# Optimization experiments

Hardware: AMD Instinct MI355X
Metric: run time of the kernel (lower is better)

The kernel has to match this reference:

```python
import jax, jax.numpy as jnp
import numpy as np

NUM_HEADS = 8
SR = 8
EPS = 1e-5


def _ln(x, g, b):
    m = jnp.mean(x, axis=-1, keepdims=True)
    v = jnp.mean((x - m) ** 2, axis=-1, keepdims=True)
    return (x - m) * jax.lax.rsqrt(v + EPS) * g + b


def _conv(x, w, b, stride, pad, groups=1):
    y = jax.lax.conv_general_dilated(
        x, w, (stride, stride), ((pad, pad), (pad, pad)),
        feature_group_count=groups,
        dimension_numbers=('NCHW', 'OIHW', 'NCHW'))
    return y + b[None, :, None, None]


def setup_inputs() -> dict:
    key = jax.random.key(0)
    ks = jax.random.split(key, 12)
    B, H, W, C = 2, 128, 128, 128
    N = H * W
    Ch = C // 2

    def nrm(k, shape, std=0.02):
        return jax.random.normal(k, shape, jnp.float32) * std

    return dict(
        x=jax.random.normal(ks[0], (B, N, C), jnp.float32),
        q_w=nrm(ks[1], (C, C)),
        sr1_w=nrm(ks[2], (C, C, 8, 8), float(np.sqrt(2.0 / (8 * 8 * C)))),
        sr1_b=jnp.zeros((C,), jnp.float32),
        norm1_g=jnp.ones((C,), jnp.float32),
        norm1_b=jnp.zeros((C,), jnp.float32),
        sr2_w=nrm(ks[3], (C, C, 4, 4), float(np.sqrt(2.0 / (4 * 4 * C)))),
        sr2_b=jnp.zeros((C,), jnp.float32),
        norm2_g=jnp.ones((C,), jnp.float32),
        norm2_b=jnp.zeros((C,), jnp.float32),
        kv1_w=nrm(ks[4], (C, C)),
        kv2_w=nrm(ks[5], (C, C)),
        lc1_w=nrm(ks[6], (Ch, 1, 3, 3), float(np.sqrt(2.0 / 9))),
        lc1_b=jnp.zeros((Ch,), jnp.float32),
        lc2_w=nrm(ks[7], (Ch, 1, 3, 3), float(np.sqrt(2.0 / 9))),
        lc2_b=jnp.zeros((Ch,), jnp.float32),
        proj_w=nrm(ks[8], (C, C)),
        proj_b=jnp.zeros((C,), jnp.float32),
        H=H, W=W,
    )


def reference(x, q_w, sr1_w, sr1_b, norm1_g, norm1_b, sr2_w, sr2_b, norm2_g,
              norm2_b, kv1_w, kv2_w, lc1_w, lc1_b, lc2_w, lc2_b, proj_w,
              proj_b, H, W):
    B, N, C = x.shape
    h = NUM_HEADS
    hd = C // h
    hh = h // 2
    Ch = C // 2
    scale = hd ** (-0.5)

    # q: (B, h, N, hd)
    q = (x @ q_w.T).reshape(B, N, h, hd).transpose(0, 2, 1, 3)
    x_img = x.transpose(0, 2, 1).reshape(B, C, H, W)

    def branch(q_half, sr_w, sr_b, ng, nb, kv_w, lc_w, lc_b, k_sr, hk, wk):
        # spatial reduction conv (kernel == stride == k_sr)
        xr = _conv(x_img, sr_w, sr_b, k_sr, 0)            # (B, C, hk, wk)
        Nk = hk * wk
        xr = xr.reshape(B, C, Nk).transpose(0, 2, 1)       # (B, Nk, C)
        xr = jax.nn.gelu(_ln(xr, ng, nb), approximate=False)
        kv = (xr @ kv_w.T).reshape(B, Nk, 2, hh, hd).transpose(2, 0, 3, 1, 4)
        k_, v_ = kv[0], kv[1]                              # (B, hh, Nk, hd)
        attn = jax.nn.softmax(
            jnp.einsum('bhqd,bhkd->bhqk', q_half, k_) * scale, axis=-1)
        # depthwise local conv fused into V
        v_img = v_.transpose(0, 2, 1, 3).reshape(B, Nk, Ch)
        v_img = v_img.transpose(0, 2, 1).reshape(B, Ch, hk, wk)
        loc = _conv(v_img, lc_w, lc_b, 1, 1, groups=Ch)
        loc = loc.reshape(B, Ch, Nk).reshape(B, hh, hd, Nk).transpose(0, 1, 3, 2)
        v_ = v_ + loc
        out = jnp.einsum('bhqk,bhkd->bhqd', attn, v_)      # (B, hh, N, hd)
        return out.transpose(0, 2, 1, 3).reshape(B, N, Ch)

    x1 = branch(q[:, :hh], sr1_w, sr1_b, norm1_g, norm1_b, kv1_w, lc1_w,
                lc1_b, SR, H // SR, W // SR)
    x2 = branch(q[:, hh:], sr2_w, sr2_b, norm2_g, norm2_b, kv2_w, lc2_w,
                lc2_b, SR // 2, H * 2 // SR, W * 2 // SR)
    out = jnp.concatenate([x1, x2], axis=-1) @ proj_w.T + proj_b
    return out
```

## Files before the change

kernel.cpp:

```cpp
#include <hip/hip_runtime.h>
#include <math.h>


typedef __attribute__((ext_vector_type(8))) short bf16x8;
typedef __attribute__((ext_vector_type(4))) float f32x4;

__device__ inline unsigned short f2bf(float f) {
  unsigned int u = __builtin_bit_cast(unsigned int, f);
  u = (u + 0x7FFFu + ((u >> 16) & 1u)) >> 16;
  return (unsigned short)u;
}

__global__ void k_cvt(const float* __restrict__ in, unsigned short* __restrict__ o, int n8) {
  int t = blockIdx.x * 256 + threadIdx.x;
  if (t >= n8) return;
  const float4 a = ((const float4*)in)[t * 2];
  const float4 b = ((const float4*)in)[t * 2 + 1];
  ((ushort4*)o)[t * 2]     = make_ushort4(f2bf(a.x), f2bf(a.y), f2bf(a.z), f2bf(a.w));
  ((ushort4*)o)[t * 2 + 1] = make_ushort4(f2bf(b.x), f2bf(b.y), f2bf(b.z), f2bf(b.w));
}

__global__ void k_cvtw4(const float* w0, const float* w1, const float* w2, const float* w3,
                        unsigned short* o0, unsigned short* o1, unsigned short* o2, unsigned short* o3) {
  const float* s; unsigned short* d;
  switch (blockIdx.y) {
    case 0: s = w0; d = o0; break;
    case 1: s = w1; d = o1; break;
    case 2: s = w2; d = o2; break;
    default: s = w3; d = o3; break;
  }
  int t = blockIdx.x * 256 + threadIdx.x;
  const float4 a = ((const float4*)s)[t * 2];
  const float4 b = ((const float4*)s)[t * 2 + 1];
  ((ushort4*)d)[t * 2]     = make_ushort4(f2bf(a.x), f2bf(a.y), f2bf(a.z), f2bf(a.w));
  ((ushort4*)d)[t * 2 + 1] = make_ushort4(f2bf(b.x), f2bf(b.y), f2bf(b.z), f2bf(b.w));
}

template <int KLOG, int SSLOG>
__global__ void k_convw(const float* __restrict__ w, unsigned short* __restrict__ o) {
  int idx = blockIdx.x * 256 + threadIdx.x;
  int k = idx & ((1 << KLOG) - 1), n = idx >> KLOG;
  int c_in = k & 127, kpos = k >> 7;
  o[idx] = f2bf(w[(n << KLOG) + (c_in << SSLOG) + kpos]);
}

template <int S, bool SPLITK, bool OUTBF, bool BIAS>
__global__ void __launch_bounds__(256)
k_mgemm(const void* __restrict__ Ap, const unsigned short* __restrict__ Bw,
        const float* __restrict__ bias, void* __restrict__ outp,
        int M, int K, int Kc) {
  constexpr int WK = (S == 8) ? 16 : 32;
  constexpr int WLOG = (S == 8) ? 4 : 5;
  constexpr int PSH = (S == 8) ? 8 : 10;
  constexpr int SLOG = (S == 8) ? 3 : 2;

  __shared__ unsigned short As[128][72];
  __shared__ unsigned short Bs[128][72];

  const int tid = threadIdx.x;
  const int lane = tid & 63, wv = tid >> 6;
  const int lq = lane & 15, g = lane >> 4;
  const int wr = wv >> 1, wc = wv & 1;
  const int m0 = blockIdx.x * 128;
  int k_begin = 0, k_end = K;
  if (SPLITK) { k_begin = blockIdx.y * Kc; k_end = k_begin + Kc; }

  const f32x4 zf = {0.f, 0.f, 0.f, 0.f};
  f32x4 acc[4][4];
#pragma unroll
  for (int i = 0; i < 4; ++i)
#pragma unroll
    for (int j = 0; j < 4; ++j) acc[i][j] = zf;

  for (int k0 = k_begin; k0 < k_end; k0 += 64) {
    __syncthreads();
    if constexpr (S == 0) {
      const unsigned short* Ab = (const unsigned short*)Ap;
      int mrow = tid >> 3, kk = (tid & 7) * 8;
#pragma unroll
      for (int p = 0; p < 4; ++p) {
        int m = p * 32 + mrow;
        *(bf16x8*)&As[m][kk] = *(const bf16x8*)(Ab + (size_t)(m0 + m) * K + k0 + kk);
      }
    } else {
      const float* xg = (const float*)Ap;
      int mrow = tid >> 4, kk = (tid & 15) * 4;
      int kgl = k0 + kk;
      int c_in = kgl & 127, kpos = kgl >> 7;
      int ky = kpos >> SLOG, kx = kpos & (S - 1);
#pragma unroll
      for (int p = 0; p < 8; ++p) {
        int m = p * 16 + mrow;
        int r = m0 + m;
        int pix = r & ((1 << PSH) - 1), bb = r >> PSH;
        int oy = pix >> WLOG, ox = pix & (WK - 1);
        int y = oy * S + ky, xx = ox * S + kx;
        const float4 v = *(const float4*)(xg + ((size_t)((bb << 14) + (y << 7) + xx) << 7) + c_in);
        *(ushort4*)&As[m][kk] = make_ushort4(f2bf(v.x), f2bf(v.y), f2bf(v.z), f2bf(v.w));
      }
    }
    {
      int nrow = tid >> 3, kk = (tid & 7) * 8;
#pragma unroll
      for (int p = 0; p < 4; ++p) {
        int n = p * 32 + nrow;
        *(bf16x8*)&Bs[n][kk] = *(const bf16x8*)(Bw + (size_t)n * K + k0 + kk);
      }
    }
    __syncthreads();
#pragma unroll
    for (int kk = 0; kk < 64; kk += 32) {
      bf16x8 af[4], bfr[4];
#pragma unroll
      for (int i = 0; i < 4; ++i) {
        af[i]  = *(const bf16x8*)&As[wr * 64 + i * 16 + lq][kk + g * 8];
        bfr[i] = *(const bf16x8*)&Bs[wc * 64 + i * 16 + lq][kk + g * 8];
      }
#pragma unroll
      for (int i = 0; i < 4; ++i)
#pragma unroll
        for (int j = 0; j < 4; ++j)
          acc[i][j] = __builtin_amdgcn_mfma_f32_16x16x32_bf16(af[i], bfr[j], acc[i][j], 0, 0, 0);
    }
  }

  size_t obase = 0;
  if (SPLITK) obase = (size_t)blockIdx.y * M * 128;
#pragma unroll
  for (int i = 0; i < 4; ++i) {
#pragma unroll
    for (int j = 0; j < 4; ++j) {
      int col = wc * 64 + j * 16 + lq;
      float bv = BIAS ? bias[col] : 0.f;
#pragma unroll
      for (int r = 0; r < 4; ++r) {
        int row = m0 + wr * 64 + i * 16 + g * 4 + r;
        float v = acc[i][j][r] + bv;
        if (OUTBF) ((unsigned short*)outp)[obase + (size_t)row * 128 + col] = f2bf(v);
        else       ((float*)outp)[obase + (size_t)row * 128 + col] = v;
      }
    }
  }
}

__global__ void __launch_bounds__(128)
k_ln_gelu(const float* __restrict__ part, int SK, int Mstride,
          const float* __restrict__ cb, const float* __restrict__ g,
          const float* __restrict__ b, unsigned short* __restrict__ out) {
  __shared__ float red[2];
  __shared__ float red2[2];
  int row = blockIdx.x;
  int t = threadIdx.x;
  const float* p = part + (size_t)row * 128 + t;
  float v = 0.f;
  for (int sk = 0; sk < SK; ++sk) v += p[(size_t)sk * Mstride];
  v += cb[t];

  float s = v;
#pragma unroll
  for (int o = 32; o > 0; o >>= 1) s += __shfl_down(s, o);
  if ((t & 63) == 0) red[t >> 6] = s;
  __syncthreads();
  float mean = (red[0] + red[1]) * (1.f / 128.f);

  float d = v - mean;
  float s2 = d * d;
#pragma unroll
  for (int o = 32; o > 0; o >>= 1) s2 += __shfl_down(s2, o);
  if ((t & 63) == 0) red2[t >> 6] = s2;
  __syncthreads();
  float var = (red2[0] + red2[1]) * (1.f / 128.f);

  float y = d * rsqrtf(var + 1e-5f) * g[t] + b[t];
  out[(size_t)row * 128 + t] = f2bf(y * 0.5f * (1.f + erff(y * 0.70710678118654752f)));
}

template <int WK>
__global__ void __launch_bounds__(256)
k_locconv(const float* __restrict__ kvb, const float* __restrict__ lw,
          const float* __restrict__ lb, float* __restrict__ vf) {
  constexpr int LOG = (WK == 16) ? 4 : 5;
  int idx = blockIdx.x * 256 + threadIdx.x;
  int c = idx & 63;
  int r = idx >> 6;
  int x = r & (WK - 1);
  int t2 = r >> LOG;
  int y = t2 & (WK - 1);
  int b = t2 >> LOG;
  const float* base = kvb + ((size_t)b * WK * WK) * 128 + 64 + c;
  float a = lb[c];
#pragma unroll
  for (int dy = -1; dy <= 1; ++dy) {
    int yy = y + dy;
    if (yy < 0 || yy >= WK) continue;
#pragma unroll
    for (int dx = -1; dx <= 1; ++dx) {
      int xx = x + dx;
      if (xx < 0 || xx >= WK) continue;
      a += base[(yy * WK + xx) * 128] * lw[c * 9 + (dy + 1) * 3 + (dx + 1)];
    }
  }
  vf[(size_t)r * 64 + c] = base[(y * WK + x) * 128] + a;
}

__global__ void __launch_bounds__(256)
k_mattn(const unsigned short* __restrict__ qb, const float* __restrict__ kvb,
        const float* __restrict__ vfb, unsigned short* __restrict__ concat,
        int NK, int h0) {
  __shared__ unsigned short Ks[64][24];
  __shared__ unsigned short Vt[16][72];
  __shared__ unsigned short Pl[4][16][40];

  const int tid = threadIdx.x;
  const int lane = tid & 63, wv = tid >> 6;
  const int lq = lane & 15, g = lane >> 4;
  const int lh = blockIdx.y, b = blockIdx.z;
  const int qbase = blockIdx.x * 64 + wv * 16;
  const int kcol = lh * 16;
  const int ocol = (h0 + lh) * 16;
  const size_t bNK = (size_t)b * NK;

  const bf16x8 kz = {0, 0, 0, 0, 0, 0, 0, 0};
  const f32x4 zf = {0.f, 0.f, 0.f, 0.f};

  bf16x8 qf = kz;
  if (g < 2)
    qf = *(const bf16x8*)(qb + ((size_t)b * 16384 + qbase + lq) * 128 + ocol + g * 8);

  f32x4 acc = zf;
  float m = -1e30f, l = 0.f;

  for (int key0 = 0; key0 < NK; key0 += 64) {
    __syncthreads();
    {
      int key = tid >> 2, hdc = (tid & 3) * 4;
      const float4 kf = *(const float4*)(kvb + (bNK + key0 + key) * 128 + kcol + hdc);
      *(ushort4*)&Ks[key][hdc] = make_ushort4(f2bf(kf.x * 0.25f), f2bf(kf.y * 0.25f),
                                              f2bf(kf.z * 0.25f), f2bf(kf.w * 0.25f));
    }
    {
      int d = tid & 15, kc = (tid >> 4) * 4;
      const float* vp = vfb + (bNK + key0 + kc) * 64 + kcol + d;
      *(ushort4*)&Vt[d][kc] = make_ushort4(f2bf(vp[0]), f2bf(vp[64]),
                                           f2bf(vp[128]), f2bf(vp[192]));
    }
    __syncthreads();

#pragma unroll
    for (int half = 0; half < 2; ++half) {
      bf16x8 k0f = kz, k1f = kz;
      if (g < 2) {
        k0f = *(const bf16x8*)&Ks[half * 32 + lq][g * 8];
        k1f = *(const bf16x8*)&Ks[half * 32 + 16 + lq][g * 8];
      }
      f32x4 c0 = __builtin_amdgcn_mfma_f32_16x16x32_bf16(k0f, qf, zf, 0, 0, 0);
      f32x4 c1 = __builtin_amdgcn_mfma_f32_16x16x32_bf16(k1f, qf, zf, 0, 0, 0);

      float tmax = fmaxf(fmaxf(fmaxf(c0[0], c0[1]), fmaxf(c0[2], c0[3])),
                         fmaxf(fmaxf(c1[0], c1[1]), fmaxf(c1[2], c1[3])));
      tmax = fmaxf(tmax, __shfl_xor(tmax, 16));
      tmax = fmaxf(tmax, __shfl_xor(tmax, 32));
      float mnew = fmaxf(m, tmax);
      float corr = __expf(m - mnew);
      float p0[4], p1[4], ls = 0.f;
#pragma unroll
      for (int r = 0; r < 4; ++r) {
        p0[r] = __expf(c0[r] - mnew);
        p1[r] = __expf(c1[r] - mnew);
        ls += p0[r] + p1[r];
      }
      ls += __shfl_xor(ls, 16);
      ls += __shfl_xor(ls, 32);
      l = l * corr + ls;
      m = mnew;
      acc = acc * corr;

      *(ushort2*)&Pl[wv][lq][g * 4]          = make_ushort2(f2bf(p0[0]), f2bf(p0[1]));
      *(ushort2*)&Pl[wv][lq][g * 4 + 2]      = make_ushort2(f2bf(p0[2]), f2bf(p0[3]));
      *(ushort2*)&Pl[wv][lq][16 + g * 4]     = make_ushort2(f2bf(p1[0]), f2bf(p1[1]));
      *(ushort2*)&Pl[wv][lq][16 + g * 4 + 2] = make_ushort2(f2bf(p1[2]), f2bf(p1[3]));

      bf16x8 pf  = *(const bf16x8*)&Pl[wv][lq][g * 8];
      bf16x8 vfr = *(const bf16x8*)&Vt[lq][half * 32 + g * 8];
      acc = __builtin_amdgcn_mfma_f32_16x16x32_bf16(vfr, pf, acc, 0, 0, 0);
    }
  }

  float inv = 1.f / l;
  size_t orow = ((size_t)b * 16384 + qbase + lq) * 128 + ocol + g * 4;
  *(ushort4*)&concat[orow] = make_ushort4(f2bf(acc[0] * inv), f2bf(acc[1] * inv),
                                          f2bf(acc[2] * inv), f2bf(acc[3] * inv));
}

extern "C" void kernel_launch(void* const* d_in, const int* in_sizes, int n_in,
                              void* d_out, int out_size, void* d_ws, size_t ws_size,
                              hipStream_t stream) {
  const float* x      = (const float*)d_in[0];
  const float* q_w    = (const float*)d_in[1];
  const float* sr1_w  = (const float*)d_in[2];
  const float* sr1_b  = (const float*)d_in[3];
  const float* n1g    = (const float*)d_in[4];
  const float* n1b    = (const float*)d_in[5];
  const float* sr2_w  = (const float*)d_in[6];
  const float* sr2_b  = (const float*)d_in[7];
  const float* n2g    = (const float*)d_in[8];
  const float* n2b    = (const float*)d_in[9];
  const float* kv1_w  = (const float*)d_in[10];
  const float* kv2_w  = (const float*)d_in[11];
  const float* lc1_w  = (const float*)d_in[12];
  const float* lc1_b  = (const float*)d_in[13];
  const float* lc2_w  = (const float*)d_in[14];
  const float* lc2_b  = (const float*)d_in[15];
  const float* proj_w = (const float*)d_in[16];
  const float* proj_b = (const float*)d_in[17];
  float* out = (float*)d_out;
  float* ws  = (float*)d_ws;

  unsigned short* xb    = (unsigned short*)(ws + 0);
  unsigned short* qbuf  = (unsigned short*)(ws + 2097152);
  unsigned short* conc  = (unsigned short*)(ws + 4194304);
  unsigned short* wBq   = (unsigned short*)(ws + 6291456);
  unsigned short* wBkv1 = (unsigned short*)(ws + 6299648);
  unsigned short* wBkv2 = (unsigned short*)(ws + 6307840);
  unsigned short* wBpj  = (unsigned short*)(ws + 6316032);
  unsigned short* wB1   = (unsigned short*)(ws + 6324224);
  unsigned short* wB2   = (unsigned short*)(ws + 6848512);
  unsigned short* xr1   = (unsigned short*)(ws + 6979584);
  unsigned short* xr2   = (unsigned short*)(ws + 7012352);
  float* kv1b  = ws + 7143424;
  float* kv2b  = ws + 7208960;
  float* vf1   = ws + 7471104;
  float* vf2   = ws + 7503872;
  float* part1 = ws + 7634944;
  float* part2 = ws + 9732096;

  k_cvt<<<2048, 256, 0, stream>>>(x, xb, 524288);
  k_cvtw4<<<dim3(8, 4), 256, 0, stream>>>(q_w, kv1_w, kv2_w, proj_w, wBq, wBkv1, wBkv2, wBpj);
  k_convw<13, 6><<<4096, 256, 0, stream>>>(sr1_w, wB1);
  k_convw<11, 4><<<1024, 256, 0, stream>>>(sr2_w, wB2);

  k_mgemm<0, false, true, false><<<dim3(256, 1), 256, 0, stream>>>(xb, wBq, nullptr, qbuf, 32768, 128, 0);

  k_mgemm<8, true, false, false><<<dim3(4, 32), 256, 0, stream>>>(x, wB1, nullptr, part1, 512, 8192, 256);
  k_mgemm<4, true, false, false><<<dim3(16, 8), 256, 0, stream>>>(x, wB2, nullptr, part2, 2048, 2048, 256);

  k_ln_gelu<<<512, 128, 0, stream>>>(part1, 32, 65536, sr1_b, n1g, n1b, xr1);
  k_ln_gelu<<<2048, 128, 0, stream>>>(part2, 8, 262144, sr2_b, n2g, n2b, xr2);

  k_mgemm<0, false, false, false><<<dim3(4, 1), 256, 0, stream>>>(xr1, wBkv1, nullptr, kv1b, 512, 128, 0);
  k_mgemm<0, false, false, false><<<dim3(16, 1), 256, 0, stream>>>(xr2, wBkv2, nullptr, kv2b, 2048, 128, 0);

  k_locconv<16><<<128, 256, 0, stream>>>(kv1b, lc1_w, lc1_b, vf1);
  k_locconv<32><<<512, 256, 0, stream>>>(kv2b, lc2_w, lc2_b, vf2);

  k_mattn<<<dim3(256, 4, 2), 256, 0, stream>>>(qbuf, kv1b, vf1, conc, 256, 0);
  k_mattn<<<dim3(256, 4, 2), 256, 0, stream>>>(qbuf, kv2b, vf2, conc, 1024, 4);

  k_mgemm<0, false, false, true><<<dim3(256, 1), 256, 0, stream>>>(conc, wBpj, proj_b, out, 32768, 128, 0);
}
```

Before: 265.2 us.

## Pre-convert K/V to bf16 head-major layout and drop LDS staging in attention

Adds a prep kernel that converts K (pre-scaled by softmax scale and log2e) and the transposed V into bf16, head-major buffers. The attention kernel then reads these operands straight from global memory without LDS staging or block barriers, runs the softmax once per 64-key tile using exp2, and is templated on the key count. Separately, the split-K factor of the two spatial-reduction conv GEMMs is doubled, producing more partial sums for the LN/GELU reduction, and float-to-bf16 conversion now uses the HIP intrinsic. Costs are two extra launches, extra workspace, and more repeated global/L2 reads of K/V across blocks.

```diff
diff --git a/kernel.cpp b/kernel.cpp
--- a/kernel.cpp
+++ b/kernel.cpp
@@ -1,15 +1,16 @@
 #include <hip/hip_runtime.h>
-#include <math.h>
+#include <hip/hip_bf16.h>
 
 
 typedef __attribute__((ext_vector_type(8))) short bf16x8;
 typedef __attribute__((ext_vector_type(4))) float f32x4;
 
 __device__ inline unsigned short f2bf(float f) {
-  unsigned int u = __builtin_bit_cast(unsigned int, f);
-  u = (u + 0x7FFFu + ((u >> 16) & 1u)) >> 16;
-  return (unsigned short)u;
-}
+  __hip_bfloat16 h = __float2bfloat16(f);
+  return __builtin_bit_cast(unsigned short, h);
+}
+
+__device__ inline float fexp2(float x) { return __builtin_amdgcn_exp2f(x); }
 
 __global__ void k_cvt(const float* __restrict__ in, unsigned short* __restrict__ o, int n8) {
   int t = blockIdx.x * 256 + threadIdx.x;
@@ -203,22 +204,41 @@
   vf[(size_t)r * 64 + c] = base[(y * WK + x) * 128] + a;
 }
 
+template <int LOGNK>
 __global__ void __launch_bounds__(256)
-k_mattn(const unsigned short* __restrict__ qb, const float* __restrict__ kvb,
-        const float* __restrict__ vfb, unsigned short* __restrict__ concat,
-        int NK, int h0) {
-  __shared__ unsigned short Ks[64][24];
-  __shared__ unsigned short Vt[16][72];
-  __shared__ unsigned short Pl[4][16][40];
+k_prep(const float* __restrict__ kvb, const float* __restrict__ vfb,
+       unsigned short* __restrict__ Kbf, unsigned short* __restrict__ Vtb) {
+  constexpr int NK = 1 << LOGNK;
+  const float SC = 0.25f * 1.44269504088896f;
+  int t = blockIdx.x * 256 + threadIdx.x;
+  if (t < (NK << 7)) {
+    int d = t & 15, key = (t >> 4) & (NK - 1);
+    int h = (t >> (4 + LOGNK)) & 3, b = t >> (6 + LOGNK);
+    Kbf[t] = f2bf(kvb[((size_t)b * NK + key) * 128 + h * 16 + d] * SC);
+  } else {
+    int v = t - (NK << 7);
+    int key = v & (NK - 1), d = (v >> LOGNK) & 15;
+    int h = (v >> (LOGNK + 4)) & 3, b = v >> (LOGNK + 6);
+    Vtb[v] = f2bf(vfb[((size_t)b * NK + key) * 64 + h * 16 + d]);
+  }
+}
+
+template <int NK>
+__global__ void __launch_bounds__(256)
+k_mattn2(const unsigned short* __restrict__ qb, const unsigned short* __restrict__ Kbf,
+         const unsigned short* __restrict__ Vtb, unsigned short* __restrict__ concat,
+         int h0) {
+  __shared__ unsigned short Pl[4][16][68];
 
   const int tid = threadIdx.x;
   const int lane = tid & 63, wv = tid >> 6;
   const int lq = lane & 15, g = lane >> 4;
   const int lh = blockIdx.y, b = blockIdx.z;
   const int qbase = blockIdx.x * 64 + wv * 16;
-  const int kcol = lh * 16;
   const int ocol = (h0 + lh) * 16;
-  const size_t bNK = (size_t)b * NK;
+
+  const unsigned short* Kh = Kbf + (size_t)(b * 4 + lh) * NK * 16;
+  const unsigned short* Vh = Vtb + ((size_t)(b * 4 + lh) * 16 + lq) * NK;
 
   const bf16x8 kz = {0, 0, 0, 0, 0, 0, 0, 0};
   const f32x4 zf = {0.f, 0.f, 0.f, 0.f};
@@ -231,57 +251,48 @@
   float m = -1e30f, l = 0.f;
 
   for (int key0 = 0; key0 < NK; key0 += 64) {
-    __syncthreads();
-    {
-      int key = tid >> 2, hdc = (tid & 3) * 4;
-      const float4 kf = *(const float4*)(kvb + (bNK + key0 + key) * 128 + kcol + hdc);
-      *(ushort4*)&Ks[key][hdc] = make_ushort4(f2bf(kf.x * 0.25f), f2bf(kf.y * 0.25f),
-                                              f2bf(kf.z * 0.25f), f2bf(kf.w * 0.25f));
-    }
-    {
-      int d = tid & 15, kc = (tid >> 4) * 4;
-      const float* vp = vfb + (bNK + key0 + kc) * 64 + kcol + d;
-      *(ushort4*)&Vt[d][kc] = make_ushort4(f2bf(vp[0]), f2bf(vp[64]),
-                                           f2bf(vp[128]), f2bf(vp[192]));
-    }
-    __syncthreads();
+    bf16x8 kf[4];
+#pragma unroll
+    for (int f = 0; f < 4; ++f)
+      kf[f] = (g < 2) ? *(const bf16x8*)(Kh + (size_t)(key0 + f * 16 + lq) * 16 + g * 8) : kz;
+    f32x4 c[4];
+#pragma unroll
+    for (int f = 0; f < 4; ++f)
+      c[f] = __builtin_amdgcn_mfma_f32_16x16x32_bf16(kf[f], qf, zf, 0, 0, 0);
+
+    float tmax = c[0][0];
+#pragma unroll
+    for (int f = 0; f < 4; ++f)
+#pragma unroll
+      for (int r = 0; r < 4; ++r) tmax = fmaxf(tmax, c[f][r]);
+    tmax = fmaxf(tmax, __shfl_xor(tmax, 16));
+    tmax = fmaxf(tmax, __shfl_xor(tmax, 32));
+    float mnew = fmaxf(m, tmax);
+    float corr = fexp2(m - mnew);
+    float p[16], ls = 0.f;
+#pragma unroll
+    for (int f = 0; f < 4; ++f)
+#pragma unroll
+      for (int r = 0; r < 4; ++r) {
+        p[f * 4 + r] = fexp2(c[f][r] - mnew);
+        ls += p[f * 4 + r];
+      }
+    ls += __shfl_xor(ls, 16);
+    ls += __shfl_xor(ls, 32);
+    l = l * corr + ls;
+    m = mnew;
+    acc *= corr;
+
+#pragma unroll
+    for (int f = 0; f < 4; ++f) {
+      *(ushort2*)&Pl[wv][lq][f * 16 + g * 4]     = make_ushort2(f2bf(p[f * 4]), f2bf(p[f * 4 + 1]));
+      *(ushort2*)&Pl[wv][lq][f * 16 + g * 4 + 2] = make_ushort2(f2bf(p[f * 4 + 2]), f2bf(p[f * 4 + 3]));
+    }
 
 #pragma unroll
     for (int half = 0; half < 2; ++half) {
-      bf16x8 k0f = kz, k1f = kz;
-      if (g < 2) {
-        k0f = *(const bf16x8*)&Ks[half * 32 + lq][g * 8];
-        k1f = *(const bf16x8*)&Ks[half * 32 + 16 + lq][g * 8];
-      }
-      f32x4 c0 = __builtin_amdgcn_mfma_f32_16x16x32_bf16(k0f, qf, zf, 0, 0, 0);
-      f32x4 c1 = __builtin_amdgcn_mfma_f32_16x16x32_bf16(k1f, qf, zf, 0, 0, 0);
-
-      float tmax = fmaxf(fmaxf(fmaxf(c0[0], c0[1]), fmaxf(c0[2], c0[3])),
-                         fmaxf(fmaxf(c1[0], c1[1]), fmaxf(c1[2], c1[3])));
-      tmax = fmaxf(tmax, __shfl_xor(tmax, 16));
-      tmax = fmaxf(tmax, __shfl_xor(tmax, 32));
-      float mnew = fmaxf(m, tmax);
-      float corr = __expf(m - mnew);
-      float p0[4], p1[4], ls = 0.f;
-#pragma unroll
-      for (int r = 0; r < 4; ++r) {
-        p0[r] = __expf(c0[r] - mnew);
-        p1[r] = __expf(c1[r] - mnew);
-        ls += p0[r] + p1[r];
-      }
-      ls += __shfl_xor(ls, 16);
-      ls += __shfl_xor(ls, 32);
-      l = l * corr + ls;
-      m = mnew;
-      acc = acc * corr;
-
-      *(ushort2*)&Pl[wv][lq][g * 4]          = make_ushort2(f2bf(p0[0]), f2bf(p0[1]));
-      *(ushort2*)&Pl[wv][lq][g * 4 + 2]      = make_ushort2(f2bf(p0[2]), f2bf(p0[3]));
-      *(ushort2*)&Pl[wv][lq][16 + g * 4]     = make_ushort2(f2bf(p1[0]), f2bf(p1[1]));
-      *(ushort2*)&Pl[wv][lq][16 + g * 4 + 2] = make_ushort2(f2bf(p1[2]), f2bf(p1[3]));
-
-      bf16x8 pf  = *(const bf16x8*)&Pl[wv][lq][g * 8];
-      bf16x8 vfr = *(const bf16x8*)&Vt[lq][half * 32 + g * 8];
+      bf16x8 pf  = *(const bf16x8*)&Pl[wv][lq][half * 32 + g * 8];
+      bf16x8 vfr = *(const bf16x8*)(Vh + key0 + half * 32 + g * 8);
       acc = __builtin_amdgcn_mfma_f32_16x16x32_bf16(vfr, pf, acc, 0, 0, 0);
     }
   }
@@ -331,8 +342,12 @@
   float* kv2b  = ws + 7208960;
   float* vf1   = ws + 7471104;
   float* vf2   = ws + 7503872;
-  float* part1 = ws + 7634944;
-  float* part2 = ws + 9732096;
+  unsigned short* Kbf1 = (unsigned short*)(ws + 7634944);
+  unsigned short* Vtb1 = (unsigned short*)(ws + 7651328);
+  unsigned short* Kbf2 = (unsigned short*)(ws + 7667712);
+  unsigned short* Vtb2 = (unsigned short*)(ws + 7733248);
+  float* part1 = ws + 7798784;
+  float* part2 = ws + 11993088;
 
   k_cvt<<<2048, 256, 0, stream>>>(x, xb, 524288);
   k_cvtw4<<<dim3(8, 4), 256, 0, stream>>>(q_w, kv1_w, kv2_w, proj_w, wBq, wBkv1, wBkv2, wBpj);
@@ -341,11 +356,11 @@
 
   k_mgemm<0, false, true, false><<<dim3(256, 1), 256, 0, stream>>>(xb, wBq, nullptr, qbuf, 32768, 128, 0);
 
-  k_mgemm<8, true, false, false><<<dim3(4, 32), 256, 0, stream>>>(x, wB1, nullptr, part1, 512, 8192, 256);
-  k_mgemm<4, true, false, false><<<dim3(16, 8), 256, 0, stream>>>(x, wB2, nullptr, part2, 2048, 2048, 256);
-
-  k_ln_gelu<<<512, 128, 0, stream>>>(part1, 32, 65536, sr1_b, n1g, n1b, xr1);
-  k_ln_gelu<<<2048, 128, 0, stream>>>(part2, 8, 262144, sr2_b, n2g, n2b, xr2);
+  k_mgemm<8, true, false, false><<<dim3(4, 64), 256, 0, stream>>>(x, wB1, nullptr, part1, 512, 8192, 128);
+  k_mgemm<4, true, false, false><<<dim3(16, 16), 256, 0, stream>>>(x, wB2, nullptr, part2, 2048, 2048, 128);
+
+  k_ln_gelu<<<512, 128, 0, stream>>>(part1, 64, 65536, sr1_b, n1g, n1b, xr1);
+  k_ln_gelu<<<2048, 128, 0, stream>>>(part2, 16, 262144, sr2_b, n2g, n2b, xr2);
 
   k_mgemm<0, false, false, false><<<dim3(4, 1), 256, 0, stream>>>(xr1, wBkv1, nullptr, kv1b, 512, 128, 0);
   k_mgemm<0, false, false, false><<<dim3(16, 1), 256, 0, stream>>>(xr2, wBkv2, nullptr, kv2b, 2048, 128, 0);
@@ -353,8 +368,11 @@
   k_locconv<16><<<128, 256, 0, stream>>>(kv1b, lc1_w, lc1_b, vf1);
   k_locconv<32><<<512, 256, 0, stream>>>(kv2b, lc2_w, lc2_b, vf2);
 
-  k_mattn<<<dim3(256, 4, 2), 256, 0, stream>>>(qbuf, kv1b, vf1, conc, 256, 0);
-  k_mattn<<<dim3(256, 4, 2), 256, 0, stream>>>(qbuf, kv2b, vf2, conc, 1024, 4);
+  k_prep<8><<<256, 256, 0, stream>>>(kv1b, vf1, Kbf1, Vtb1);
+  k_prep<10><<<1024, 256, 0, stream>>>(kv2b, vf2, Kbf2, Vtb2);
+
+  k_mattn2<256><<<dim3(256, 4, 2), 256, 0, stream>>>(qbuf, Kbf1, Vtb1, conc, 0);
+  k_mattn2<1024><<<dim3(256, 4, 2), 256, 0, stream>>>(qbuf, Kbf2, Vtb2, conc, 4);
 
   k_mgemm<0, false, false, true><<<dim3(256, 1), 256, 0, stream>>>(conc, wBpj, proj_b, out, 32768, 128, 0);
 }
```

Measured after the change: 255.7 us. 1.04x faster.
